# Optimization experiments

Measured on AMD Instinct MI355X. Metric: run time of the kernel, lower is better.

Reference implementation:

```python
import jax, jax.numpy as jnp
import numpy as np

N = 50000
E = 800000
F = 64
HID = 64
HEADS = 4
NTYPES = 3


def layer_norm(x, g, b, eps=1e-5):
    mu = x.mean(-1, keepdims=True)
    var = ((x - mu) ** 2).mean(-1, keepdims=True)
    return (x - mu) * jax.lax.rsqrt(var + eps) * g + b


def gat_conv(x, src, dst, n, W, att_src, att_dst, bias, concat):
    # PyG GATConv: per-head linear transform, additive attention, segment softmax over dst.
    H, C = att_src.shape
    xp = (x @ W).reshape(n, H, C)                       # [N,H,C]
    a_s = (xp * att_src).sum(-1)                         # [N,H]
    a_d = (xp * att_dst).sum(-1)                         # [N,H]
    e = jax.nn.leaky_relu(a_s[src] + a_d[dst], 0.2)      # [Etot,H]
    m = jax.ops.segment_max(e, dst, num_segments=n)      # stable softmax per target
    ex = jnp.exp(e - m[dst])
    denom = jax.ops.segment_sum(ex, dst, num_segments=n)
    alpha = ex / (denom[dst] + 1e-16)                    # [Etot,H]
    msg = xp[src] * alpha[:, :, None]                    # [Etot,H,C]
    out = jax.ops.segment_sum(msg, dst, num_segments=n)  # [N,H,C]
    out = out.reshape(n, H * C) if concat else out.mean(1)
    return out + bias


def setup_inputs() -> dict:
    key = jax.random.key(0)
    ks = jax.random.split(key, 12)
    f32 = jnp.float32
    return {
        'node_features': jax.random.normal(ks[0], (N, F), f32),
        'node_types': jax.random.randint(ks[1], (N,), 0, NTYPES),
        'edge_index': jax.random.randint(ks[2], (2, E), 0, N),
        'type_emb': jax.random.normal(ks[3], (NTYPES, HID), f32) * 0.02,
        'proj_W': jax.random.normal(ks[4], (F, HID), f32) / np.sqrt(F).astype(np.float32),
        'proj_b': jnp.zeros((HID,), f32),
        'W0': jax.random.normal(ks[5], (HID, HEADS * HID), f32) / np.sqrt(HID).astype(np.float32),
        'att_src0': jax.random.normal(ks[6], (HEADS, HID), f32) * 0.1,
        'att_dst0': jax.random.normal(ks[7], (HEADS, HID), f32) * 0.1,
        'bias0': jnp.zeros((HEADS * HID,), f32),
        'ln0_g': jnp.ones((HEADS * HID,), f32),
        'ln0_b': jnp.zeros((HEADS * HID,), f32),
        'W1': jax.random.normal(ks[8], (HEADS * HID, HEADS * HID), f32) / np.sqrt(HEADS * HID).astype(np.float32),
        'att_src1': jax.random.normal(ks[9], (HEADS, HID), f32) * 0.1,
        'att_dst1': jax.random.normal(ks[10], (HEADS, HID), f32) * 0.1,
        'bias1': jnp.zeros((HID,), f32),
        'ln1_g': jnp.ones((HID,), f32),
        'ln1_b': jnp.zeros((HID,), f32),
    }


def reference(node_features, node_types, edge_index, type_emb, proj_W, proj_b,
              W0, att_src0, att_dst0, bias0, ln0_g, ln0_b,
              W1, att_src1, att_dst1, bias1, ln1_g, ln1_b):
    n = node_features.shape[0]
    loop = jnp.arange(n)
    src = jnp.concatenate([edge_index[0], loop])  # add_self_loops=True (PyG default)
    dst = jnp.concatenate([edge_index[1], loop])
    # input projection + node-type embedding
    x = node_features @ proj_W + proj_b + type_emb[node_types]
    # layer 0: concat heads -> [N, HEADS*HID]
    h = gat_conv(x, src, dst, n, W0, att_src0, att_dst0, bias0, True)
    h = jax.nn.relu(layer_norm(h, ln0_g, ln0_b))  # dropout is identity in eval
    # layer 1: mean over heads -> [N, HID]; residual skipped (shape mismatch 256 vs 64)
    h2 = gat_conv(h, src, dst, n, W1, att_src1, att_dst1, bias1, False)
    h2 = jax.nn.relu(layer_norm(h2, ln1_g, ln1_b))
    return h2
```

## Files before the change

### kernel.cpp

```cpp
#include <hip/hip_runtime.h>
#include <hip/hip_bf16.h>
#include <hip/hip_fp16.h>

typedef unsigned short u16;
typedef unsigned int u32;
typedef short s16x8 __attribute__((ext_vector_type(8)));
typedef float f32x4 __attribute__((ext_vector_type(4)));

__device__ __forceinline__ float bf2f(u16 u) {
  return __uint_as_float(((u32)u) << 16);
}

__device__ __forceinline__ u16 f2b(float f) {
  __hip_bfloat16 h = __float2bfloat16(f);
  return *(u16*)&h;
}

__device__ __forceinline__ u32 packbf(float lo, float hi) {
  return (u32)f2b(lo) | ((u32)f2b(hi) << 16);
}

__device__ __forceinline__ bool sniff_bf16(const void* ones) {
  u32 w = *(const u32*)ones;
  return (w >> 16) == (w & 0xFFFFu);
}

__device__ __forceinline__ float ldf(const void* p, size_t i, bool bf) {
  return bf ? bf2f(((const u16*)p)[i]) : ((const float*)p)[i];
}

__device__ __forceinline__ float rdlane_f(float v, int e) {
  return __uint_as_float((u32)__builtin_amdgcn_readlane((int)__float_as_uint(v), e));
}

__global__ __launch_bounds__(256) void deg_count_k(const int* __restrict__ ei, int E, int N,
                                                   int* __restrict__ deg) {
  int i = blockIdx.x * 256 + threadIdx.x;
  if (i >= E + N) return;
  int d = (i < E) ? ei[E + i] : (i - E);
  atomicAdd(deg + d, 1);
}

__global__ __launch_bounds__(256) void scan_local_k(const int* __restrict__ deg,
                                                    int* __restrict__ off,
                                                    int* __restrict__ bsum, int N) {
  __shared__ int ps[256];
  int t = threadIdx.x;
  int i = blockIdx.x * 256 + t;
  int v = (i < N) ? deg[i] : 0;
  ps[t] = v;
  __syncthreads();
#pragma unroll
  for (int o = 1; o < 256; o <<= 1) {
    int u = (t >= o) ? ps[t - o] : 0;
    __syncthreads();
    ps[t] += u;
    __syncthreads();
  }
  if (i < N) off[i] = ps[t] - v;
  if (t == 255) bsum[blockIdx.x] = ps[255];
}

__global__ __launch_bounds__(256) void scan_add2_k(int* __restrict__ off,
                                                   const int* __restrict__ bsum,
                                                   int* __restrict__ cur,
                                                   int N, int Etot, int nb) {
  __shared__ int red[256];
  int t = threadIdx.x;
  int b = blockIdx.x;
  red[t] = (t < nb && t < b) ? bsum[t] : 0;
  __syncthreads();
#pragma unroll
  for (int o = 128; o > 0; o >>= 1) {
    if (t < o) red[t] += red[t + o];
    __syncthreads();
  }
  int pre = red[0];
  int i = b * 256 + t;
  if (i == 0) off[N] = Etot;
  if (i >= N) return;
  int o2 = off[i] + pre;
  off[i] = o2;
  cur[i] = o2;
}

__global__ __launch_bounds__(256) void scatter_k(const int* __restrict__ ei, int E, int N,
                                                 int* __restrict__ cur, int* __restrict__ csr) {
  int i = blockIdx.x * 256 + threadIdx.x;
  if (i >= E + N) return;
  int s, d;
  if (i < E) { s = ei[i]; d = ei[E + i]; } else { s = i - E; d = s; }
  int p = atomicAdd(cur + d, 1);
  csr[p] = s;
}

__global__ __launch_bounds__(256) void prep_k(
    const void* __restrict__ W0, const void* __restrict__ W1,
    const void* __restrict__ pW, const void* __restrict__ atts,
    const void* __restrict__ attd, const void* __restrict__ pb,
    const void* __restrict__ temb, const void* __restrict__ ones,
    u16* __restrict__ Wp0, u16* __restrict__ Wp1, u16* __restrict__ Wpp,
    u16* __restrict__ Wpe, float* __restrict__ ca) {
  bool bf = sniff_bf16(ones);
  int b = blockIdx.x;
  int t = threadIdx.x;
  if (b < 320) {
    const void* W = (b < 64) ? W0 : W1;
    u16* Wp = (b < 64) ? Wp0 : Wp1;
    int i = (b < 64 ? b : b - 64) * 256 + t;
    int j = i & 7;
    int q = (i >> 3) & 3;
    int c = (i >> 5) & 255;
    int kc = i >> 13;
    int k = kc * 32 + q * 8 + j;
    Wp[i] = f2b(ldf(W, (size_t)k * 256 + c, bf));
  } else if (b < 336) {
    int i = (b - 320) * 256 + t;
    int j = i & 7;
    int q = (i >> 3) & 3;
    int c = (i >> 5) & 63;
    int kc = i >> 11;
    int k = kc * 32 + q * 8 + j;
    Wpp[i] = f2b(ldf(pW, (size_t)k * 64 + c, bf));
  } else {
    __shared__ float va[256], vd[256];
    int h = t >> 6, k = t & 63;
    {
      float s = 0.f, d = 0.f;
      for (int c = 0; c < 64; c++) {
        float w = ldf(W0, (size_t)k * 256 + h * 64 + c, bf);
        s += w * ldf(atts, h * 64 + c, bf);
        d += w * ldf(attd, h * 64 + c, bf);
      }
      va[t] = s;
      vd[t] = d;
    }
    __syncthreads();
    {
      int i = k;
      float wa = 0.f, wd = 0.f;
      for (int kk = 0; kk < 64; kk++) {
        float wv = ldf(pW, (size_t)i * 64 + kk, bf);
        wa += wv * va[h * 64 + kk];
        wd += wv * vd[h * 64 + kk];
      }
      int kc = i >> 5, q = (i >> 3) & 3, j = i & 7;
      Wpe[((kc * 16 + h) * 4 + q) * 8 + j] = f2b(wa);
      Wpe[((kc * 16 + 4 + h) * 4 + q) * 8 + j] = f2b(wd);
    }
    Wpe[256 + t] = 0;
    Wpe[768 + t] = 0;
    if (t < 12) {
      int ty = t >> 2, hh = t & 3;
      float sa = 0.f, sd = 0.f;
      for (int kk = 0; kk < 64; kk++) {
        float bv = ldf(pb, kk, bf) + ldf(temb, ty * 64 + kk, bf);
        sa += bv * va[hh * 64 + kk];
        sd += bv * vd[hh * 64 + kk];
      }
      ca[t] = sa;
      ca[12 + t] = sd;
    }
  }
}

__global__ __launch_bounds__(256) void proj2_k(
    const void* __restrict__ nf, const int* __restrict__ ntype,
    const u16* __restrict__ Wpp, const u16* __restrict__ Wpe,
    const void* __restrict__ pbias, const void* __restrict__ temb,
    const float* __restrict__ ca, const void* __restrict__ ones,
    u16* __restrict__ x, float* __restrict__ aS, float* __restrict__ aD, int N) {
  bool bf = sniff_bf16(ones);
  int t = threadIdx.x;
  int wave = t >> 6, lane = t & 63;
  int r = lane & 15, q = lane >> 4;
  int row0 = blockIdx.x * 16;
  int arow = row0 + r;
  if (arow >= N) arow = N - 1;
  f32x4 xacc = {0.f, 0.f, 0.f, 0.f};
  f32x4 eacc = {0.f, 0.f, 0.f, 0.f};
#pragma unroll
  for (int kc = 0; kc < 2; kc++) {
    s16x8 a;
    if (bf) {
      a = *(const s16x8*)((const u16*)nf + (size_t)arow * 64 + kc * 32 + q * 8);
    } else {
      const float* fp = (const float*)nf + (size_t)arow * 64 + kc * 32 + q * 8;
#pragma unroll
      for (int j = 0; j < 8; j++) a[j] = (short)f2b(fp[j]);
    }
    {
      int c = wave * 16 + r;
      s16x8 b = *(const s16x8*)(Wpp + (((size_t)kc * 64 + c) * 4 + q) * 8);
      xacc = __builtin_amdgcn_mfma_f32_16x16x32_bf16(a, b, xacc, 0, 0, 0);
    }
    if (wave == 3) {
      s16x8 b = *(const s16x8*)(Wpe + (((size_t)kc * 16 + r) * 4 + q) * 8);
      eacc = __builtin_amdgcn_mfma_f32_16x16x32_bf16(a, b, eacc, 0, 0, 0);
    }
  }
#pragma unroll
  for (int rg = 0; rg < 4; rg++) {
    int row = row0 + q * 4 + rg;
    if (row >= N) continue;
    int col = wave * 16 + r;
    int ty = ntype[row];
    float v = xacc[rg] + ldf(pbias, col, bf) + ldf(temb, ty * 64 + col, bf);
    x[(size_t)row * 64 + col] = f2b(v);
    if (wave == 3 && r < 8) {
      if (r < 4) aS[(size_t)row * 4 + r] = eacc[rg] + ca[ty * 4 + r];
      else       aD[(size_t)row * 4 + (r - 4)] = eacc[rg] + ca[12 + ty * 4 + (r - 4)];
    }
  }
}

__global__ __launch_bounds__(256) void l0g1f_k(
    const int* __restrict__ off, const int* __restrict__ csr,
    const float* __restrict__ aS0, const float* __restrict__ aD0,
    const u16* __restrict__ x, const u16* __restrict__ Wp0,
    const void* __restrict__ bias0, const void* __restrict__ g0,
    const void* __restrict__ be0, const u16* __restrict__ Wp1,
    const void* __restrict__ atts, const void* __restrict__ attd,
    const void* __restrict__ ones,
    u16* __restrict__ C, float* __restrict__ aS1, float* __restrict__ aD1, int N) {
  bool bf = sniff_bf16(ones);
  __shared__ u16 ag[16][264];
  __shared__ u16 hs[16][264];
  __shared__ float sm_s[4][16], sm_q[4][16];
  int t = threadIdx.x;
  int wave = t >> 6, lane = t & 63;
  int r = lane & 15, q = lane >> 4;
  int row0 = blockIdx.x * 16;
  const u16* xl = x + lane;
  for (int jj = 0; jj < 4; jj++) {
    int lr = wave * 4 + jj;
    int n = row0 + lr;
    float den[4] = {0.f, 0.f, 0.f, 0.f};
    float acc[4] = {0.f, 0.f, 0.f, 0.f};
    if (n < N) {
      int start = off[n], end = off[n + 1];
      float4 ad4 = *(const float4*)(aD0 + (size_t)n * 4);
      float ad[4] = {ad4.x, ad4.y, ad4.z, ad4.w};
      for (int cs = start; cs < end; cs += 64) {
        int cnt = end - cs; if (cnt > 64) cnt = 64;
        int s = 0;
        float ex[4] = {0.f, 0.f, 0.f, 0.f};
        if (lane < cnt) {
          s = csr[cs + lane];
          float4 as4 = *(const float4*)(aS0 + (size_t)s * 4);
          float av[4] = {as4.x, as4.y, as4.z, as4.w};
#pragma unroll
          for (int h = 0; h < 4; h++) {
            float v = av[h] + ad[h];
            v = (v > 0.f ? v : 0.2f * v) - 3.0f;
            ex[h] = __expf(v);
            den[h] += ex[h];
          }
        }
#pragma unroll 8
        for (int e = 0; e < cnt; e++) {
          int se = __builtin_amdgcn_readlane(s, e);
          float w0 = rdlane_f(ex[0], e);
          float w1 = rdlane_f(ex[1], e);
          float w2 = rdlane_f(ex[2], e);
          float w3 = rdlane_f(ex[3], e);
          float xv = bf2f(xl[(size_t)se * 64]);
          acc[0] += w0 * xv;
          acc[1] += w1 * xv;
          acc[2] += w2 * xv;
          acc[3] += w3 * xv;
        }
      }
#pragma unroll
      for (int h = 0; h < 4; h++) {
#pragma unroll
        for (int o = 32; o > 0; o >>= 1) den[h] += __shfl_xor(den[h], o, 64);
        acc[h] /= (den[h] + 1e-16f);
      }
    }
#pragma unroll
    for (int h = 0; h < 4; h++) ag[lr][h * 64 + lane] = f2b(acc[h]);
  }
  __syncthreads();
  {
    f32x4 acc[4] = {{0.f, 0.f, 0.f, 0.f}, {0.f, 0.f, 0.f, 0.f},
                    {0.f, 0.f, 0.f, 0.f}, {0.f, 0.f, 0.f, 0.f}};
#pragma unroll
    for (int kc = 0; kc < 2; kc++) {
      s16x8 a = *(const s16x8*)&ag[r][wave * 64 + kc * 32 + q * 8];
#pragma unroll
      for (int ct = 0; ct < 4; ct++) {
        int c = wave * 64 + ct * 16 + r;
        s16x8 b = *(const s16x8*)(Wp0 + (((size_t)kc * 256 + c) * 4 + q) * 8);
        acc[ct] = __builtin_amdgcn_mfma_f32_16x16x32_bf16(a, b, acc[ct], 0, 0, 0);
      }
    }
    float yv[4][4];
    float s_p[4] = {0.f, 0.f, 0.f, 0.f};
    float q_p[4] = {0.f, 0.f, 0.f, 0.f};
#pragma unroll
    for (int ct = 0; ct < 4; ct++) {
      float bc = ldf(bias0, wave * 64 + ct * 16 + r, bf);
#pragma unroll
      for (int rg = 0; rg < 4; rg++) {
        float y = acc[ct][rg] + bc;
        yv[ct][rg] = y;
        s_p[rg] += y;
        q_p[rg] += y * y;
      }
    }
#pragma unroll
    for (int o = 1; o < 16; o <<= 1) {
#pragma unroll
      for (int rg = 0; rg < 4; rg++) {
        s_p[rg] += __shfl_xor(s_p[rg], o, 64);
        q_p[rg] += __shfl_xor(q_p[rg], o, 64);
      }
    }
    if (r == 0) {
#pragma unroll
      for (int rg = 0; rg < 4; rg++) {
        sm_s[wave][q * 4 + rg] = s_p[rg];
        sm_q[wave][q * 4 + rg] = q_p[rg];
      }
    }
    __syncthreads();
#pragma unroll
    for (int rg = 0; rg < 4; rg++) {
      int lr = q * 4 + rg;
      float mu = (sm_s[0][lr] + sm_s[1][lr] + sm_s[2][lr] + sm_s[3][lr]) * (1.f / 256.f);
      float vq = (sm_q[0][lr] + sm_q[1][lr] + sm_q[2][lr] + sm_q[3][lr]) * (1.f / 256.f) - mu * mu;
      float inv = rsqrtf(vq + 1e-5f);
#pragma unroll
      for (int ct = 0; ct < 4; ct++) {
        int c = wave * 64 + ct * 16 + r;
        float o_ = (yv[ct][rg] - mu) * inv * ldf(g0, c, bf) + ldf(be0, c, bf);
        hs[lr][c] = f2b(fmaxf(o_, 0.f));
      }
    }
  }
  __syncthreads();
  int colw = wave * 64;
  f32x4 acc[4] = {{0.f, 0.f, 0.f, 0.f}, {0.f, 0.f, 0.f, 0.f},
                  {0.f, 0.f, 0.f, 0.f}, {0.f, 0.f, 0.f, 0.f}};
#pragma unroll
  for (int kc = 0; kc < 8; kc++) {
    s16x8 a = *(const s16x8*)&hs[r][kc * 32 + q * 8];
#pragma unroll
    for (int ct = 0; ct < 4; ct++) {
      int c = colw + ct * 16 + r;
      s16x8 b = *(const s16x8*)(Wp1 + (((size_t)kc * 256 + c) * 4 + q) * 8);
      acc[ct] = __builtin_amdgcn_mfma_f32_16x16x32_bf16(a, b, acc[ct], 0, 0, 0);
    }
  }
#pragma unroll
  for (int ct = 0; ct < 4; ct++) {
#pragma unroll
    for (int rg = 0; rg < 4; rg++) {
      int row = row0 + q * 4 + rg;
      if (row < N) C[(size_t)row * 256 + colw + ct * 16 + r] = f2b(acc[ct][rg]);
    }
  }
  float sp[4] = {0.f, 0.f, 0.f, 0.f};
  float dp[4] = {0.f, 0.f, 0.f, 0.f};
#pragma unroll
  for (int ct = 0; ct < 4; ct++) {
    int c = colw + ct * 16 + r;
    float av = ldf(atts, c, bf);
    float dv = ldf(attd, c, bf);
#pragma unroll
    for (int rg = 0; rg < 4; rg++) {
      sp[rg] += acc[ct][rg] * av;
      dp[rg] += acc[ct][rg] * dv;
    }
  }
#pragma unroll
  for (int o = 1; o < 16; o <<= 1) {
#pragma unroll
    for (int rg = 0; rg < 4; rg++) {
      sp[rg] += __shfl_xor(sp[rg], o, 64);
      dp[rg] += __shfl_xor(dp[rg], o, 64);
    }
  }
  if (r == 0) {
#pragma unroll
    for (int rg = 0; rg < 4; rg++) {
      int row = row0 + q * 4 + rg;
      if (row < N) {
        aS1[(size_t)row * 4 + wave] = sp[rg];
        aD1[(size_t)row * 4 + wave] = dp[rg];
      }
    }
  }
}

__global__ __launch_bounds__(256) void agg1_k(
    const int* __restrict__ off, const int* __restrict__ csr,
    const float* __restrict__ aS, const float* __restrict__ aD,
    const u16* __restrict__ xp,
    const void* __restrict__ bias, const void* __restrict__ g,
    const void* __restrict__ b, void* __restrict__ out, int N) {
  bool bf = sniff_bf16(g);
  int n = blockIdx.x * 4 + (threadIdx.x >> 6);
  int lane = threadIdx.x & 63;
  if (n >= N) return;
  int start = off[n], end = off[n + 1];
  bool hiSel = (lane & 32) != 0;
  float4 ad4 = *(const float4*)(aD + (size_t)n * 4);
  float ad[4] = {ad4.x, ad4.y, ad4.z, ad4.w};
  float den[4] = {0.f, 0.f, 0.f, 0.f};
  float acc[4] = {0.f, 0.f, 0.f, 0.f};
  const u32* xp32 = (const u32*)xp;

  for (int cs = start; cs < end; cs += 64) {
    int cnt = end - cs; if (cnt > 64) cnt = 64;
    int s = 0;
    float ex[4] = {0.f, 0.f, 0.f, 0.f};
    if (lane < cnt) {
      s = csr[cs + lane];
      float4 as4 = *(const float4*)(aS + (size_t)s * 4);
      float av[4] = {as4.x, as4.y, as4.z, as4.w};
#pragma unroll
      for (int h = 0; h < 4; h++) {
        float v = av[h] + ad[h];
        v = (v > 0.f ? v : 0.2f * v) - 3.0f;
        ex[h] = __expf(v);
        den[h] += ex[h];
      }
    }
#pragma unroll 8
    for (int e = 0; e < cnt; e++) {
      int se = __builtin_amdgcn_readlane(s, e);
      float w0 = rdlane_f(ex[0], e);
      float w1 = rdlane_f(ex[1], e);
      float w2 = rdlane_f(ex[2], e);
      float w3 = rdlane_f(ex[3], e);
      float wA = hiSel ? w1 : w0;
      float wB = hiSel ? w3 : w2;
      const u32* xr = xp32 + (size_t)se * 128 + lane;
      u32 dA = xr[0];
      u32 dB = xr[64];
      acc[0] += wA * __uint_as_float(dA << 16);
      acc[1] += wA * __uint_as_float(dA & 0xffff0000u);
      acc[2] += wB * __uint_as_float(dB << 16);
      acc[3] += wB * __uint_as_float(dB & 0xffff0000u);
    }
  }
#pragma unroll
  for (int h = 0; h < 4; h++) {
#pragma unroll
    for (int o = 32; o > 0; o >>= 1) den[h] += __shfl_xor(den[h], o, 64);
  }
  {
    float dA = (hiSel ? den[1] : den[0]) + 1e-16f;
    float dB = (hiSel ? den[3] : den[2]) + 1e-16f;
    acc[0] /= dA; acc[1] /= dA;
    acc[2] /= dB; acc[3] /= dB;
  }
  float p0 = acc[0] + acc[2];
  float p1 = acc[1] + acc[3];
  p0 += __shfl_xor(p0, 32, 64);
  p1 += __shfl_xor(p1, 32, 64);
  int c = 2 * (lane & 31);
  float z0 = 0.25f * p0 + ldf(bias, c, bf);
  float z1 = 0.25f * p1 + ldf(bias, c + 1, bf);
  float sum = z0 + z1;
#pragma unroll
  for (int o = 32; o > 0; o >>= 1) sum += __shfl_xor(sum, o, 64);
  float mu = sum * (1.f / 128.f);
  float d0 = z0 - mu, d1 = z1 - mu;
  float sq = d0 * d0 + d1 * d1;
#pragma unroll
  for (int o = 32; o > 0; o >>= 1) sq += __shfl_xor(sq, o, 64);
  float inv = rsqrtf(sq * (1.f / 128.f) + 1e-5f);
  float y0 = fmaxf(d0 * inv * ldf(g, c, bf) + ldf(b, c, bf), 0.f);
  float y1 = fmaxf(d1 * inv * ldf(g, c + 1, bf) + ldf(b, c + 1, bf), 0.f);
  if (lane < 32) {
    if (bf) {
      ((u32*)out)[(size_t)n * 32 + lane] = packbf(y0, y1);
    } else {
      ((float2*)out)[(size_t)n * 32 + lane] = make_float2(y0, y1);
    }
  }
}

extern "C" void kernel_launch(void* const* d_in, const int* in_sizes, int n_in,
                              void* d_out, int out_size, void* d_ws, size_t ws_size,
                              hipStream_t stream) {
  const void* nf   = d_in[0];
  const int* ntyp  = (const int*)d_in[1];
  const int* ei    = (const int*)d_in[2];
  const void* temb = d_in[3];
  const void* pW   = d_in[4];
  const void* pb   = d_in[5];
  const void* W0   = d_in[6];
  const void* as0  = d_in[7];
  const void* ad0  = d_in[8];
  const void* b0   = d_in[9];
  const void* g0   = d_in[10];
  const void* be0  = d_in[11];
  const void* W1   = d_in[12];
  const void* as1  = d_in[13];
  const void* ad1  = d_in[14];
  const void* b1   = d_in[15];
  const void* g1   = d_in[16];
  const void* be1  = d_in[17];

  int N = in_sizes[0] / 64;
  int E = in_sizes[2] / 2;
  int Etot = E + N;

  u16* Wp0 = (u16*)d_ws;
  u16* Wp1 = Wp0 + 64 * 256;
  u16* Wpp = Wp1 + 256 * 256;
  u16* Wpe = Wpp + 64 * 64;
  u16* xb  = Wpe + 1024;
  u16* A   = xb + (size_t)N * 64;
  float* aS0b = (float*)(A + (size_t)N * 256);
  float* aD0b = aS0b + (size_t)N * 4;
  float* aS1b = aD0b + (size_t)N * 4;
  float* aD1b = aS1b + (size_t)N * 4;
  float* ca = aD1b + (size_t)N * 4;
  int* deg  = (int*)(ca + 32);
  int* off  = deg + N;
  int* csr  = off + N + 1;
  int* bsum = csr + Etot;

  dim3 b256(256);
  int nodeBlocks = (N + 3) / 4;
  int edgeBlocksT = (Etot + 255) / 256;
  int gemmBlocks = (N + 15) / 16;
  int scanBlocks = (N + 255) / 256;

  hipMemsetAsync(deg, 0, (size_t)N * sizeof(int), stream);
  deg_count_k<<<edgeBlocksT, b256, 0, stream>>>(ei, E, N, deg);
  scan_local_k<<<scanBlocks, b256, 0, stream>>>(deg, off, bsum, N);
  scan_add2_k<<<scanBlocks, b256, 0, stream>>>(off, bsum, deg, N, Etot, scanBlocks);
  scatter_k<<<edgeBlocksT, b256, 0, stream>>>(ei, E, N, deg, csr);
  prep_k<<<337, b256, 0, stream>>>(W0, W1, pW, as0, ad0, pb, temb, g0,
                                   Wp0, Wp1, Wpp, Wpe, ca);

  proj2_k<<<gemmBlocks, b256, 0, stream>>>(nf, ntyp, Wpp, Wpe, pb, temb, ca, g0,
                                           xb, aS0b, aD0b, N);
  l0g1f_k<<<gemmBlocks, b256, 0, stream>>>(off, csr, aS0b, aD0b, xb, Wp0, b0, g0, be0,
                                           Wp1, as1, ad1, g0, A, aS1b, aD1b, N);
  agg1_k<<<nodeBlocks, b256, 0, stream>>>(off, csr, aS1b, aD1b, A, b1, g1, be1, d_out, N);
}
```

Baseline: 429.3 us.

## Split layer-0 aggregation out of fused GEMM kernel into separate node-parallel kernel

The layer-0 attention aggregation moves out of the fused aggregation+GEMM kernel into its own kernel, agg0_k, with one wave per node. Its result is written to a new global bf16 buffer of N×256, which the GEMM kernel then reads instead of shared memory. Previously each wave handled four nodes one after another, and the whole block waited at a barrier before the MFMA stage, so uneven node degrees serialized work. The split adds a global round trip of about 25 MB and an extra launch in exchange for more parallelism and better load balance in the gather.

```diff
diff --git a/kernel.cpp b/kernel.cpp
--- a/kernel.cpp
+++ b/kernel.cpp
@@ -214,80 +214,83 @@
   }
 }
 
-__global__ __launch_bounds__(256) void l0g1f_k(
+__global__ __launch_bounds__(256) void agg0_k(
     const int* __restrict__ off, const int* __restrict__ csr,
-    const float* __restrict__ aS0, const float* __restrict__ aD0,
-    const u16* __restrict__ x, const u16* __restrict__ Wp0,
+    const float* __restrict__ aS, const float* __restrict__ aD,
+    const u16* __restrict__ x, u16* __restrict__ Ag, int N) {
+  int n = blockIdx.x * 4 + (threadIdx.x >> 6);
+  int lane = threadIdx.x & 63;
+  if (n >= N) return;
+  int start = off[n], end = off[n + 1];
+  float4 ad4 = *(const float4*)(aD + (size_t)n * 4);
+  float ad[4] = {ad4.x, ad4.y, ad4.z, ad4.w};
+  float den[4] = {0.f, 0.f, 0.f, 0.f};
+  float acc[4] = {0.f, 0.f, 0.f, 0.f};
+  const u16* xl = x + lane;
+
+  for (int cs = start; cs < end; cs += 64) {
+    int cnt = end - cs; if (cnt > 64) cnt = 64;
+    int s = 0;
+    float ex[4] = {0.f, 0.f, 0.f, 0.f};
+    if (lane < cnt) {
+      s = csr[cs + lane];
+      float4 as4 = *(const float4*)(aS + (size_t)s * 4);
+      float av[4] = {as4.x, as4.y, as4.z, as4.w};
+#pragma unroll
+      for (int h = 0; h < 4; h++) {
+        float v = av[h] + ad[h];
+        v = (v > 0.f ? v : 0.2f * v) - 3.0f;
+        ex[h] = __expf(v);
+        den[h] += ex[h];
+      }
+    }
+#pragma unroll 8
+    for (int e = 0; e < cnt; e++) {
+      int se = __builtin_amdgcn_readlane(s, e);
+      float w0 = rdlane_f(ex[0], e);
+      float w1 = rdlane_f(ex[1], e);
+      float w2 = rdlane_f(ex[2], e);
+      float w3 = rdlane_f(ex[3], e);
+      float xv = bf2f(xl[(size_t)se * 64]);
+      acc[0] += w0 * xv;
+      acc[1] += w1 * xv;
+      acc[2] += w2 * xv;
+      acc[3] += w3 * xv;
+    }
+  }
+#pragma unroll
+  for (int h = 0; h < 4; h++) {
+#pragma unroll
+    for (int o = 32; o > 0; o >>= 1) den[h] += __shfl_xor(den[h], o, 64);
+    acc[h] /= (den[h] + 1e-16f);
+  }
+#pragma unroll
+  for (int h = 0; h < 4; h++) Ag[(size_t)n * 256 + h * 64 + lane] = f2b(acc[h]);
+}
+
+__global__ __launch_bounds__(256) void l0g1_k(
+    const u16* __restrict__ Ag, const u16* __restrict__ Wp0,
     const void* __restrict__ bias0, const void* __restrict__ g0,
     const void* __restrict__ be0, const u16* __restrict__ Wp1,
     const void* __restrict__ atts, const void* __restrict__ attd,
     const void* __restrict__ ones,
-    u16* __restrict__ C, float* __restrict__ aS1, float* __restrict__ aD1, int N) {
+    u16* __restrict__ C, float* __restrict__ aS, float* __restrict__ aD, int N) {
   bool bf = sniff_bf16(ones);
-  __shared__ u16 ag[16][264];
   __shared__ u16 hs[16][264];
   __shared__ float sm_s[4][16], sm_q[4][16];
   int t = threadIdx.x;
   int wave = t >> 6, lane = t & 63;
   int r = lane & 15, q = lane >> 4;
   int row0 = blockIdx.x * 16;
-  const u16* xl = x + lane;
-  for (int jj = 0; jj < 4; jj++) {
-    int lr = wave * 4 + jj;
-    int n = row0 + lr;
-    float den[4] = {0.f, 0.f, 0.f, 0.f};
-    float acc[4] = {0.f, 0.f, 0.f, 0.f};
-    if (n < N) {
-      int start = off[n], end = off[n + 1];
-      float4 ad4 = *(const float4*)(aD0 + (size_t)n * 4);
-      float ad[4] = {ad4.x, ad4.y, ad4.z, ad4.w};
-      for (int cs = start; cs < end; cs += 64) {
-        int cnt = end - cs; if (cnt > 64) cnt = 64;
-        int s = 0;
-        float ex[4] = {0.f, 0.f, 0.f, 0.f};
-        if (lane < cnt) {
-          s = csr[cs + lane];
-          float4 as4 = *(const float4*)(aS0 + (size_t)s * 4);
-          float av[4] = {as4.x, as4.y, as4.z, as4.w};
-#pragma unroll
-          for (int h = 0; h < 4; h++) {
-            float v = av[h] + ad[h];
-            v = (v > 0.f ? v : 0.2f * v) - 3.0f;
-            ex[h] = __expf(v);
-            den[h] += ex[h];
-          }
-        }
-#pragma unroll 8
-        for (int e = 0; e < cnt; e++) {
-          int se = __builtin_amdgcn_readlane(s, e);
-          float w0 = rdlane_f(ex[0], e);
-          float w1 = rdlane_f(ex[1], e);
-          float w2 = rdlane_f(ex[2], e);
-          float w3 = rdlane_f(ex[3], e);
-          float xv = bf2f(xl[(size_t)se * 64]);
-          acc[0] += w0 * xv;
-          acc[1] += w1 * xv;
-          acc[2] += w2 * xv;
-          acc[3] += w3 * xv;
-        }
-      }
-#pragma unroll
-      for (int h = 0; h < 4; h++) {
-#pragma unroll
-        for (int o = 32; o > 0; o >>= 1) den[h] += __shfl_xor(den[h], o, 64);
-        acc[h] /= (den[h] + 1e-16f);
-      }
-    }
-#pragma unroll
-    for (int h = 0; h < 4; h++) ag[lr][h * 64 + lane] = f2b(acc[h]);
-  }
-  __syncthreads();
+  int arow = row0 + r;
+  if (arow >= N) arow = N - 1;
   {
+    const u16* ap = Ag + (size_t)arow * 256 + wave * 64 + q * 8;
     f32x4 acc[4] = {{0.f, 0.f, 0.f, 0.f}, {0.f, 0.f, 0.f, 0.f},
                     {0.f, 0.f, 0.f, 0.f}, {0.f, 0.f, 0.f, 0.f}};
 #pragma unroll
     for (int kc = 0; kc < 2; kc++) {
-      s16x8 a = *(const s16x8*)&ag[r][wave * 64 + kc * 32 + q * 8];
+      s16x8 a = *(const s16x8*)(ap + kc * 32);
 #pragma unroll
       for (int ct = 0; ct < 4; ct++) {
         int c = wave * 64 + ct * 16 + r;
@@ -387,8 +390,8 @@
     for (int rg = 0; rg < 4; rg++) {
       int row = row0 + q * 4 + rg;
       if (row < N) {
-        aS1[(size_t)row * 4 + wave] = sp[rg];
-        aD1[(size_t)row * 4 + wave] = dp[rg];
+        aS[(size_t)row * 4 + wave] = sp[rg];
+        aD[(size_t)row * 4 + wave] = dp[rg];
       }
     }
   }
@@ -515,7 +518,8 @@
   u16* Wpp = Wp1 + 256 * 256;
   u16* Wpe = Wpp + 64 * 64;
   u16* xb  = Wpe + 1024;
-  u16* A   = xb + (size_t)N * 64;
+  u16* Ag  = xb + (size_t)N * 64;
+  u16* A   = Ag + (size_t)N * 256;
   float* aS0b = (float*)(A + (size_t)N * 256);
   float* aD0b = aS0b + (size_t)N * 4;
   float* aS1b = aD0b + (size_t)N * 4;
@@ -542,7 +546,8 @@
 
   proj2_k<<<gemmBlocks, b256, 0, stream>>>(nf, ntyp, Wpp, Wpe, pb, temb, ca, g0,
                                            xb, aS0b, aD0b, N);
-  l0g1f_k<<<gemmBlocks, b256, 0, stream>>>(off, csr, aS0b, aD0b, xb, Wp0, b0, g0, be0,
-                                           Wp1, as1, ad1, g0, A, aS1b, aD1b, N);
+  agg0_k<<<nodeBlocks, b256, 0, stream>>>(off, csr, aS0b, aD0b, xb, Ag, N);
+  l0g1_k<<<gemmBlocks, b256, 0, stream>>>(Ag, Wp0, b0, g0, be0, Wp1, as1, ad1, g0,
+                                          A, aS1b, aD1b, N);
   agg1_k<<<nodeBlocks, b256, 0, stream>>>(off, csr, aS1b, aD1b, A, b1, g1, be1, d_out, N);
 }
```

New measurement: 411.5 us (median of 2 runs). 4.1% less time.
